# Kernel tuning notes

Hardware: AMD Instinct MI355X
Metric: run time of the kernel (lower is better)

## Reference

```python
import jax, jax.numpy as jnp
import numpy as np

N = 100000      # nodes
E = 1600000     # edges (avg degree 16)
D_IN, D_H, D_OUT = 128, 128, 40
BN_EPS = 1e-5


def _gcn_norm(edge_index):
    # add self-loops, compute symmetric normalization D^-1/2 (A+I) D^-1/2
    loops = jnp.arange(N, dtype=edge_index.dtype)
    src = jnp.concatenate([edge_index[0], loops])
    dst = jnp.concatenate([edge_index[1], loops])
    deg = jax.ops.segment_sum(jnp.ones(src.shape[0], jnp.float32), dst, num_segments=N)
    dinv = jnp.where(deg > 0, jax.lax.rsqrt(deg), 0.0)
    norm = dinv[src] * dinv[dst]  # [E+N]
    return src, dst, norm


def _gcn_conv(h, W, b, src, dst, norm):
    h = h @ W                          # [N, d_out]
    msg = h[src] * norm[:, None]       # [E+N, d_out] gather + scale
    out = jax.ops.segment_sum(msg, dst, num_segments=N)
    return out + b


def _bn(h, g, beta, mean, var):
    return g * (h - mean) * jax.lax.rsqrt(var + BN_EPS) + beta


def setup_inputs() -> dict:
    key = jax.random.key(0)
    ks = jax.random.split(key, 16)
    x = jax.random.normal(ks[0], (N, D_IN), jnp.float32)
    edge_index = jax.random.randint(ks[1], (2, E), 0, N, dtype=jnp.int32)
    s_in, s_h = 1.0 / np.sqrt(D_IN), 1.0 / np.sqrt(D_H)
    W0 = jax.random.normal(ks[2], (D_IN, D_H), jnp.float32) * s_in
    b0 = jnp.zeros((D_H,), jnp.float32)
    W1 = jax.random.normal(ks[3], (D_H, D_H), jnp.float32) * s_h
    b1 = jnp.zeros((D_H,), jnp.float32)
    W2 = jax.random.normal(ks[4], (D_H, D_OUT), jnp.float32) * s_h
    b2 = jnp.zeros((D_OUT,), jnp.float32)
    g0 = jnp.ones((D_H,), jnp.float32)
    be0 = jnp.zeros((D_H,), jnp.float32)
    m0 = jax.random.normal(ks[5], (D_H,), jnp.float32) * 0.1
    v0 = jax.random.uniform(ks[6], (D_H,), jnp.float32) + 0.5
    g1 = jnp.ones((D_H,), jnp.float32)
    be1 = jnp.zeros((D_H,), jnp.float32)
    m1 = jax.random.normal(ks[7], (D_H,), jnp.float32) * 0.1
    v1 = jax.random.uniform(ks[8], (D_H,), jnp.float32) + 0.5
    return {"x": x, "edge_index": edge_index,
            "W0": W0, "b0": b0, "W1": W1, "b1": b1, "W2": W2, "b2": b2,
            "g0": g0, "be0": be0, "m0": m0, "v0": v0,
            "g1": g1, "be1": be1, "m1": m1, "v1": v1}


def reference(x, edge_index, W0, b0, W1, b1, W2, b2,
              g0, be0, m0, v0, g1, be1, m1, v1):
    src, dst, norm = _gcn_norm(edge_index)
    h = _gcn_conv(x, W0, b0, src, dst, norm)
    h = jax.nn.relu(_bn(h, g0, be0, m0, v0))   # dropout = identity in eval
    h = _gcn_conv(h, W1, b1, src, dst, norm)
    h = jax.nn.relu(_bn(h, g1, be1, m1, v1))
    h = _gcn_conv(h, W2, b2, src, dst, norm)
    return jax.nn.log_softmax(h, axis=1)
```

## Files before the change

### kernel.cpp

```cpp
#include <hip/hip_runtime.h>
#include <math.h>


#define CSHIFT 9
#define CSZ 512
#define PCHUNK 8192

typedef unsigned short u16;
typedef unsigned int u32;
typedef unsigned char u8;
typedef float f32x4 __attribute__((ext_vector_type(4)));
typedef short s16x8 __attribute__((ext_vector_type(8)));

__device__ inline float bflo(u32 u) { return __uint_as_float(u << 16); }
__device__ inline float bfhi(u32 u) { return __uint_as_float(u & 0xffff0000u); }
__device__ inline u16 f2bf(float f) {
    u32 b = __float_as_uint(f);
    b += 0x7fff + ((b >> 16) & 1);
    return (u16)(b >> 16);
}
__device__ inline u32 pack2(float lo, float hi) {
    return (u32)f2bf(lo) | ((u32)f2bf(hi) << 16);
}


__global__ __launch_bounds__(256) void k_hist1(const int* __restrict__ dst,
                                               int* __restrict__ hist1,
                                               int E, int NB) {
    __shared__ int h[256];
    int t = threadIdx.x;
    h[t] = 0;
    __syncthreads();
    for (int i = blockIdx.x * 256 * 16 + t; i < min(E, (blockIdx.x + 1) * 256 * 16);
         i += 256)
        atomicAdd(&h[dst[i] >> CSHIFT], 1);
    __syncthreads();
    if (t < NB && h[t]) atomicAdd(&hist1[t], h[t]);
}

__global__ __launch_bounds__(256) void k_scan1(const int* __restrict__ hist1,
                                               int* __restrict__ base1,
                                               int* __restrict__ cur1,
                                               int NB, int E) {
    __shared__ int sc[256];
    int t = threadIdx.x;
    int v = (t < NB) ? hist1[t] : 0;
    sc[t] = v;
    __syncthreads();
    for (int d = 1; d < 256; d <<= 1) {
        int add = (t >= d) ? sc[t - d] : 0;
        __syncthreads();
        sc[t] += add;
        __syncthreads();
    }
    if (t < NB) {
        int excl = sc[t] - v;
        base1[t] = excl;
        cur1[t] = excl;
    }
    if (t == 0) base1[NB] = E;
}

__global__ __launch_bounds__(256) void k_part1(const int* __restrict__ src,
                                               const int* __restrict__ dst,
                                               int* __restrict__ cur1,
                                               u32* __restrict__ bkt,
                                               int E, int NB) {
    __shared__ u32 stage[PCHUNK];
    __shared__ u8 sbin[PCHUNK];
    __shared__ int cnt[256];
    __shared__ int lbase[256];
    __shared__ int lcur[256];
    __shared__ int gb[256];
    int t = threadIdx.x;
    int base = blockIdx.x * PCHUNK;
    int n = min(PCHUNK, E - base);
    cnt[t] = 0;
    __syncthreads();
    for (int i = t; i < n; i += 256) atomicAdd(&cnt[dst[base + i] >> CSHIFT], 1);
    __syncthreads();
    int v = cnt[t];
    lbase[t] = v;
    __syncthreads();
    for (int d = 1; d < 256; d <<= 1) {
        int add = (t >= d) ? lbase[t - d] : 0;
        __syncthreads();
        lbase[t] += add;
        __syncthreads();
    }
    {
        int excl = lbase[t] - v;
        __syncthreads();
        lbase[t] = excl;
        lcur[t] = excl;
        if (t < NB && v) gb[t] = atomicAdd(&cur1[t], v);
    }
    __syncthreads();
    for (int i = t; i < n; i += 256) {
        int d = dst[base + i];
        int s = src[base + i];
        int bin = d >> CSHIFT;
        int p = atomicAdd(&lcur[bin], 1);
        stage[p] = ((u32)s << CSHIFT) | (u32)(d & (CSZ - 1));
        sbin[p] = (u8)bin;
    }
    __syncthreads();
    for (int k = t; k < n; k += 256) {
        int bin = sbin[k];
        bkt[gb[bin] + (k - lbase[bin])] = stage[k];
    }
}

__global__ __launch_bounds__(256) void k_csr(const u32* __restrict__ bkt,
                                             const int* __restrict__ base1,
                                             int* __restrict__ col,
                                             int* __restrict__ row,
                                             float* __restrict__ dinv,
                                             int N, int E) {
    __shared__ int deg[CSZ];
    __shared__ int cur[CSZ];
    __shared__ int sc[256];
    int b = blockIdx.x;
    int t = threadIdx.x;
    int start = base1[b];
    int end = base1[b + 1];
    int nbase = b << CSHIFT;
    deg[t] = 0;
    deg[t + 256] = 0;
    __syncthreads();
    for (int i = start + t; i < end; i += 256)
        atomicAdd(&deg[bkt[i] & (CSZ - 1)], 1);
    __syncthreads();
    int d0 = deg[2 * t], d1 = deg[2 * t + 1];
    int s = d0 + d1;
    sc[t] = s;
    __syncthreads();
    for (int d = 1; d < 256; d <<= 1) {
        int add = (t >= d) ? sc[t - d] : 0;
        __syncthreads();
        sc[t] += add;
        __syncthreads();
    }
    int excl = sc[t] - s;
    cur[2 * t] = excl;
    cur[2 * t + 1] = excl + d0;
    int n0 = nbase + 2 * t, n1 = n0 + 1;
    if (n0 < N) { row[n0] = start + excl;      dinv[n0] = rsqrtf((float)(d0 + 1)); }
    if (n1 < N) { row[n1] = start + excl + d0; dinv[n1] = rsqrtf((float)(d1 + 1)); }
    __syncthreads();
    for (int i = start + t; i < end; i += 256) {
        u32 v = bkt[i];
        int p = start + atomicAdd(&cur[v & (CSZ - 1)], 1);
        col[p] = (int)(v >> CSHIFT);
    }
    if (b == 0 && t == 0) row[N] = E;
}


__global__ __launch_bounds__(256) void k_packW(const float* __restrict__ W,
                                               u16* __restrict__ Wpk) {
    int g = blockIdx.x * 256 + threadIdx.x;
    int j = g & 7;
    int l = (g >> 3) & 63;
    int f = g >> 9;
    int ct = f & 7, ks = f >> 3;
    int krow = ks * 32 + ((l >> 4) << 3) + j;
    int wcol = ct * 16 + (l & 15);
    Wpk[g] = f2bf(W[krow * 128 + wcol]);
}

template <bool AFP32>
__global__ __launch_bounds__(256) void k_gemm128m(const void* __restrict__ Av,
                                                  const u16* __restrict__ Wpk,
                                                  u16* __restrict__ C,
                                                  const float* __restrict__ dinv,
                                                  int M) {
    int tid = threadIdx.x;
    int wv = blockIdx.x * 4 + (tid >> 6);
    int rowbase = wv * 16;
    if (rowbase >= M) return;
    int l = tid & 63;
    int r = l & 15, hi = l >> 4;

    f32x4 acc[8];
#pragma unroll
    for (int ct = 0; ct < 8; ++ct) acc[ct] = (f32x4)(0.f);

    const uint4* wp = (const uint4*)Wpk;
#pragma unroll
    for (int ks = 0; ks < 4; ++ks) {
        s16x8 afrag;
        int abase = (rowbase + r) * 128 + ks * 32 + hi * 8;
        if (AFP32) {
            const float* A = (const float*)Av;
            float4 a0 = *(const float4*)&A[abase];
            float4 a1 = *(const float4*)&A[abase + 4];
            u32 p0 = pack2(a0.x, a0.y), p1 = pack2(a0.z, a0.w);
            u32 p2 = pack2(a1.x, a1.y), p3 = pack2(a1.z, a1.w);
            uint4 u = make_uint4(p0, p1, p2, p3);
            afrag = *(s16x8*)&u;
        } else {
            const u16* A = (const u16*)Av;
            uint4 u = *(const uint4*)&A[abase];
            afrag = *(s16x8*)&u;
        }
#pragma unroll
        for (int ct = 0; ct < 8; ++ct) {
            uint4 b = wp[(ks * 8 + ct) * 64 + l];
            s16x8 bfrag = *(s16x8*)&b;
            acc[ct] = __builtin_amdgcn_mfma_f32_16x16x32_bf16(afrag, bfrag, acc[ct], 0, 0, 0);
        }
    }
    float dv[4];
#pragma unroll
    for (int reg = 0; reg < 4; ++reg) dv[reg] = dinv[rowbase + 4 * hi + reg];
#pragma unroll
    for (int ct = 0; ct < 8; ++ct) {
#pragma unroll
        for (int reg = 0; reg < 4; ++reg) {
            int orow = rowbase + 4 * hi + reg;
            C[(size_t)orow * 128 + ct * 16 + r] = f2bf(dv[reg] * acc[ct][reg]);
        }
    }
}

__global__ __launch_bounds__(256) void k_gemm40(const u16* __restrict__ A,
                                                const float* __restrict__ W,
                                                u16* __restrict__ C,
                                                const float* __restrict__ dinv,
                                                int M) {
    __shared__ float Ws[128 * 40];
    for (int i = threadIdx.x; i < 128 * 40; i += 256) Ws[i] = W[i];
    __syncthreads();
    int r0 = blockIdx.x * 512 + threadIdx.x;
    int r1 = r0 + 256;
    float acc0[40], acc1[40];
#pragma unroll
    for (int c = 0; c < 40; ++c) { acc0[c] = 0.f; acc1[c] = 0.f; }
    const uint2* x0 = (const uint2*)(A + (size_t)min(r0, M - 1) * 128);
    const uint2* x1 = (const uint2*)(A + (size_t)min(r1, M - 1) * 128);
    for (int kb = 0; kb < 32; ++kb) {
        uint2 ua = x0[kb];
        uint2 ub = x1[kb];
        float a0x = bflo(ua.x), a0y = bfhi(ua.x), a0z = bflo(ua.y), a0w = bfhi(ua.y);
        float a1x = bflo(ub.x), a1y = bfhi(ub.x), a1z = bflo(ub.y), a1w = bfhi(ub.y);
        const float* wr = &Ws[kb * 160];
#pragma unroll
        for (int c4 = 0; c4 < 10; ++c4) {
            float4 wk0 = *(const float4*)&wr[c4 * 4];
            float4 wk1 = *(const float4*)&wr[40 + c4 * 4];
            float4 wk2 = *(const float4*)&wr[80 + c4 * 4];
            float4 wk3 = *(const float4*)&wr[120 + c4 * 4];
            int c = c4 * 4;
            acc0[c+0] = fmaf(a0x,wk0.x, fmaf(a0y,wk1.x, fmaf(a0z,wk2.x, fmaf(a0w,wk3.x, acc0[c+0]))));
            acc0[c+1] = fmaf(a0x,wk0.y, fmaf(a0y,wk1.y, fmaf(a0z,wk2.y, fmaf(a0w,wk3.y, acc0[c+1]))));
            acc0[c+2] = fmaf(a0x,wk0.z, fmaf(a0y,wk1.z, fmaf(a0z,wk2.z, fmaf(a0w,wk3.z, acc0[c+2]))));
            acc0[c+3] = fmaf(a0x,wk0.w, fmaf(a0y,wk1.w, fmaf(a0z,wk2.w, fmaf(a0w,wk3.w, acc0[c+3]))));
            acc1[c+0] = fmaf(a1x,wk0.x, fmaf(a1y,wk1.x, fmaf(a1z,wk2.x, fmaf(a1w,wk3.x, acc1[c+0]))));
            acc1[c+1] = fmaf(a1x,wk0.y, fmaf(a1y,wk1.y, fmaf(a1z,wk2.y, fmaf(a1w,wk3.y, acc1[c+1]))));
            acc1[c+2] = fmaf(a1x,wk0.z, fmaf(a1y,wk1.z, fmaf(a1z,wk2.z, fmaf(a1w,wk3.z, acc1[c+2]))));
            acc1[c+3] = fmaf(a1x,wk0.w, fmaf(a1y,wk1.w, fmaf(a1z,wk2.w, fmaf(a1w,wk3.w, acc1[c+3]))));
        }
    }
    if (r0 < M) {
        float s = dinv[r0];
        u32* crow = (u32*)(C + (size_t)r0 * 40);
#pragma unroll
        for (int c2 = 0; c2 < 20; ++c2) crow[c2] = pack2(s * acc0[2*c2], s * acc0[2*c2+1]);
    }
    if (r1 < M) {
        float s = dinv[r1];
        u32* crow = (u32*)(C + (size_t)r1 * 40);
#pragma unroll
        for (int c2 = 0; c2 < 20; ++c2) crow[c2] = pack2(s * acc1[2*c2], s * acc1[2*c2+1]);
    }
}


__global__ __launch_bounds__(256) void k_agg128(const u16* __restrict__ X,
                                                u16* __restrict__ Y,
                                                const int* __restrict__ row,
                                                const int* __restrict__ col,
                                                const float* __restrict__ dinv,
                                                const float* __restrict__ bias,
                                                const float* __restrict__ g,
                                                const float* __restrict__ be,
                                                const float* __restrict__ mean,
                                                const float* __restrict__ var,
                                                int n) {
    int tid = threadIdx.x;
    int wid = tid >> 6, lane = tid & 63;
    int half = lane >> 5, l5 = lane & 31;
    int node = (blockIdx.x * 4 + wid) * 2 + half;
    bool valid = node < n;
    int nc = valid ? node : (n - 1);
    const uint2* xp = (const uint2*)X;
    int s = row[nc], e = row[nc + 1];
    uint2 v = xp[(size_t)nc * 32 + l5];
    float a0 = bflo(v.x), a1 = bfhi(v.x), a2 = bflo(v.y), a3 = bfhi(v.y);
    float b0 = 0, b1 = 0, b2 = 0, b3 = 0;
    float c0 = 0, c1 = 0, c2 = 0, c3 = 0;
    float d0 = 0, d1 = 0, d2 = 0, d3 = 0;
    int j = s;
    for (; j + 8 <= e; j += 8) {
        int e0 = col[j], e1 = col[j+1], e2 = col[j+2], e3 = col[j+3];
        int e4 = col[j+4], e5 = col[j+5], e6 = col[j+6], e7 = col[j+7];
        uint2 x0 = xp[(size_t)e0 * 32 + l5];
        uint2 x1 = xp[(size_t)e1 * 32 + l5];
        uint2 x2 = xp[(size_t)e2 * 32 + l5];
        uint2 x3 = xp[(size_t)e3 * 32 + l5];
        uint2 x4 = xp[(size_t)e4 * 32 + l5];
        uint2 x5 = xp[(size_t)e5 * 32 + l5];
        uint2 x6 = xp[(size_t)e6 * 32 + l5];
        uint2 x7 = xp[(size_t)e7 * 32 + l5];
        a0 += bflo(x0.x); a1 += bfhi(x0.x); a2 += bflo(x0.y); a3 += bfhi(x0.y);
        b0 += bflo(x1.x); b1 += bfhi(x1.x); b2 += bflo(x1.y); b3 += bfhi(x1.y);
        c0 += bflo(x2.x); c1 += bfhi(x2.x); c2 += bflo(x2.y); c3 += bfhi(x2.y);
        d0 += bflo(x3.x); d1 += bfhi(x3.x); d2 += bflo(x3.y); d3 += bfhi(x3.y);
        a0 += bflo(x4.x); a1 += bfhi(x4.x); a2 += bflo(x4.y); a3 += bfhi(x4.y);
        b0 += bflo(x5.x); b1 += bfhi(x5.x); b2 += bflo(x5.y); b3 += bfhi(x5.y);
        c0 += bflo(x6.x); c1 += bfhi(x6.x); c2 += bflo(x6.y); c3 += bfhi(x6.y);
        d0 += bflo(x7.x); d1 += bfhi(x7.x); d2 += bflo(x7.y); d3 += bfhi(x7.y);
    }
    for (; j + 2 <= e; j += 2) {
        int e0 = col[j], e1 = col[j+1];
        uint2 x0 = xp[(size_t)e0 * 32 + l5];
        uint2 x1 = xp[(size_t)e1 * 32 + l5];
        a0 += bflo(x0.x); a1 += bfhi(x0.x); a2 += bflo(x0.y); a3 += bfhi(x0.y);
        b0 += bflo(x1.x); b1 += bfhi(x1.x); b2 += bflo(x1.y); b3 += bfhi(x1.y);
    }
    if (j < e) {
        uint2 x0 = xp[(size_t)col[j] * 32 + l5];
        c0 += bflo(x0.x); c1 += bfhi(x0.x); c2 += bflo(x0.y); c3 += bfhi(x0.y);
    }
    float dv = dinv[nc];
    float s0 = dv * ((a0 + b0) + (c0 + d0));
    float s1 = dv * ((a1 + b1) + (c1 + d1));
    float s2 = dv * ((a2 + b2) + (c2 + d2));
    float s3 = dv * ((a3 + b3) + (c3 + d3));
    float4 g4 = ((const float4*)g)[l5];
    float4 be4 = ((const float4*)be)[l5];
    float4 m4 = ((const float4*)mean)[l5];
    float4 v4 = ((const float4*)var)[l5];
    float4 bi4 = ((const float4*)bias)[l5];
    float sc0 = g4.x * rsqrtf(v4.x + 1e-5f);
    float sc1 = g4.y * rsqrtf(v4.y + 1e-5f);
    float sc2 = g4.z * rsqrtf(v4.z + 1e-5f);
    float sc3 = g4.w * rsqrtf(v4.w + 1e-5f);
    float y0 = fmaxf(fmaf(sc0, s0, fmaf(sc0, bi4.x - m4.x, be4.x)), 0.f);
    float y1 = fmaxf(fmaf(sc1, s1, fmaf(sc1, bi4.y - m4.y, be4.y)), 0.f);
    float y2 = fmaxf(fmaf(sc2, s2, fmaf(sc2, bi4.z - m4.z, be4.z)), 0.f);
    float y3 = fmaxf(fmaf(sc3, s3, fmaf(sc3, bi4.w - m4.w, be4.w)), 0.f);
    if (valid) {
        uint2 o;
        o.x = pack2(y0, y1);
        o.y = pack2(y2, y3);
        ((uint2*)Y)[(size_t)node * 32 + l5] = o;
    }
}

__global__ __launch_bounds__(256) void k_agg40(const u16* __restrict__ X,
                                               float* __restrict__ out,
                                               const int* __restrict__ row,
                                               const int* __restrict__ col,
                                               const float* __restrict__ dinv,
                                               const float* __restrict__ b2,
                                               int n) {
    int tid = threadIdx.x;
    int wid = tid >> 6, lane = tid & 63;
    int half = lane >> 5, l5 = lane & 31;
    int node = (blockIdx.x * 4 + wid) * 2 + half;
    bool valid = node < n;
    int nc = valid ? node : (n - 1);
    bool active = l5 < 20;
    const u32* xp = (const u32*)X;
    int s = row[nc], e = row[nc + 1];
    float a0 = 0, a1 = 0, b0 = 0, b1 = 0, c0 = 0, c1 = 0, d0 = 0, d1 = 0;
    if (active) {
        u32 v = xp[(size_t)nc * 20 + l5];
        a0 = bflo(v); a1 = bfhi(v);
    }
    int j = s;
    for (; j + 8 <= e; j += 8) {
        int e0 = col[j], e1 = col[j+1], e2 = col[j+2], e3 = col[j+3];
        int e4 = col[j+4], e5 = col[j+5], e6 = col[j+6], e7 = col[j+7];
        if (active) {
            u32 x0 = xp[(size_t)e0 * 20 + l5];
            u32 x1 = xp[(size_t)e1 * 20 + l5];
            u32 x2 = xp[(size_t)e2 * 20 + l5];
            u32 x3 = xp[(size_t)e3 * 20 + l5];
            u32 x4 = xp[(size_t)e4 * 20 + l5];
            u32 x5 = xp[(size_t)e5 * 20 + l5];
            u32 x6 = xp[(size_t)e6 * 20 + l5];
            u32 x7 = xp[(size_t)e7 * 20 + l5];
            a0 += bflo(x0); a1 += bfhi(x0);
            b0 += bflo(x1); b1 += bfhi(x1);
            c0 += bflo(x2); c1 += bfhi(x2);
            d0 += bflo(x3); d1 += bfhi(x3);
            a0 += bflo(x4); a1 += bfhi(x4);
            b0 += bflo(x5); b1 += bfhi(x5);
            c0 += bflo(x6); c1 += bfhi(x6);
            d0 += bflo(x7); d1 += bfhi(x7);
        }
    }
    for (; j + 2 <= e; j += 2) {
        int e0 = col[j], e1 = col[j+1];
        if (active) {
            u32 x0 = xp[(size_t)e0 * 20 + l5];
            u32 x1 = xp[(size_t)e1 * 20 + l5];
            a0 += bflo(x0); a1 += bfhi(x0);
            b0 += bflo(x1); b1 += bfhi(x1);
        }
    }
    if (j < e && active) {
        u32 x0 = xp[(size_t)col[j] * 20 + l5];
        c0 += bflo(x0); c1 += bfhi(x0);
    }
    float dv = dinv[nc];
    float ylo = -INFINITY, yhi = -INFINITY;
    if (active) {
        float2 bb = ((const float2*)b2)[l5];
        ylo = fmaf(dv, (a0 + b0) + (c0 + d0), bb.x);
        yhi = fmaf(dv, (a1 + b1) + (c1 + d1), bb.y);
    }
    float m = fmaxf(ylo, yhi);
#pragma unroll
    for (int d = 16; d; d >>= 1) m = fmaxf(m, __shfl_xor(m, d));
    float ex = active ? (__expf(ylo - m) + __expf(yhi - m)) : 0.f;
#pragma unroll
    for (int d = 16; d; d >>= 1) ex += __shfl_xor(ex, d);
    if (valid && active) {
        float lse = m + __logf(ex);
        ((float2*)out)[(size_t)node * 20 + l5] = make_float2(ylo - lse, yhi - lse);
    }
}


extern "C" void kernel_launch(void* const* d_in, const int* in_sizes, int n_in,
                              void* d_out, int out_size, void* d_ws, size_t ws_size,
                              hipStream_t stream) {
    const float* x   = (const float*)d_in[0];
    const int*   ei  = (const int*)d_in[1];
    const float* W0  = (const float*)d_in[2];
    const float* b0  = (const float*)d_in[3];
    const float* W1  = (const float*)d_in[4];
    const float* b1  = (const float*)d_in[5];
    const float* W2  = (const float*)d_in[6];
    const float* b2  = (const float*)d_in[7];
    const float* g0  = (const float*)d_in[8];
    const float* be0 = (const float*)d_in[9];
    const float* m0  = (const float*)d_in[10];
    const float* v0  = (const float*)d_in[11];
    const float* g1  = (const float*)d_in[12];
    const float* be1 = (const float*)d_in[13];
    const float* m1  = (const float*)d_in[14];
    const float* v1  = (const float*)d_in[15];
    float* out = (float*)d_out;

    int N = in_sizes[0] / 128;
    int E = in_sizes[1] / 2;
    const int* src = ei;
    const int* dst = ei + E;

    int NB = (N + CSZ - 1) / CSZ;

    char* ws = (char*)d_ws;
    size_t off = 0;
    auto alloc = [&](size_t bytes) -> char* {
        char* p = ws + off;
        off += (bytes + 255) & ~(size_t)255;
        return p;
    };
    u16*   XsA   = (u16*)alloc((size_t)N * 128 * 2);
    u16*   hB    = (u16*)alloc((size_t)N * 128 * 2);
    u16*   bufC  = (u16*)alloc((size_t)N * 40 * 2);
    int*   col   = (int*)alloc((size_t)E * 4);
    int*   row   = (int*)alloc((size_t)(N + 1) * 4);
    float* dinv  = (float*)alloc((size_t)N * 4);
    int*   hist1 = (int*)alloc((size_t)(NB + 1) * 4);
    int*   base1 = (int*)alloc((size_t)(NB + 1) * 4);
    int*   cur1  = (int*)alloc((size_t)(NB + 1) * 4);
    u16*   Wpk0  = (u16*)alloc(128 * 128 * 2);
    u16*   Wpk1  = (u16*)alloc(128 * 128 * 2);
    u32*   bkt   = (u32*)XsA;

    hipMemsetAsync(hist1, 0, (size_t)(NB + 1) * 4, stream);
    k_hist1<<<(E + 4095) / 4096, 256, 0, stream>>>(dst, hist1, E, NB);
    k_scan1<<<1, 256, 0, stream>>>(hist1, base1, cur1, NB, E);
    k_part1<<<(E + PCHUNK - 1) / PCHUNK, 256, 0, stream>>>(src, dst, cur1, bkt, E, NB);
    k_csr<<<NB, 256, 0, stream>>>(bkt, base1, col, row, dinv, N, E);
    k_packW<<<64, 256, 0, stream>>>(W0, Wpk0);
    k_packW<<<64, 256, 0, stream>>>(W1, Wpk1);

    int gemmGrid = ((N + 15) / 16 + 3) / 4;
    k_gemm128m<true><<<gemmGrid, 256, 0, stream>>>(x, Wpk0, XsA, dinv, N);
    k_agg128<<<(N + 7) / 8, 256, 0, stream>>>(XsA, hB, row, col, dinv, b0, g0, be0, m0, v0, N);
    k_gemm128m<false><<<gemmGrid, 256, 0, stream>>>(hB, Wpk1, XsA, dinv, N);
    k_agg128<<<(N + 7) / 8, 256, 0, stream>>>(XsA, hB, row, col, dinv, b1, g1, be1, m1, v1, N);
    k_gemm40<<<(N + 511) / 512, 256, 0, stream>>>(hB, W2, bufC, dinv, N);
    k_agg40<<<(N + 7) / 8, 256, 0, stream>>>(bufC, out, row, col, dinv, b2, N);
}
```

Measured before the change: 315.7 us.

## Fuse aggregation+BN+ReLU with the following layer's GEMM via LDS-staged MFMA

Merges each 128-wide aggregation kernel with the next layer's weight GEMM. Each block aggregates 16 nodes, applies bias, BN and ReLU, writes the bf16 rows to a swizzled LDS tile, then runs MFMA on it against packed weights. This removes the round trip of the intermediate hidden matrix through global memory and two launches. The last GEMM now uses MFMA with weights zero-padded to 48 columns instead of a scalar FMA kernel. The cost is lower occupancy from 512-thread blocks with a barrier, and only some waves do the MFMA work.

Result: faster. 284.8 us (-9.8%).

```diff
diff --git a/kernel.cpp b/kernel.cpp
--- a/kernel.cpp
+++ b/kernel.cpp
@@ -169,12 +169,25 @@
     Wpk[g] = f2bf(W[krow * 128 + wcol]);
 }
 
-template <bool AFP32>
-__global__ __launch_bounds__(256) void k_gemm128m(const void* __restrict__ Av,
-                                                  const u16* __restrict__ Wpk,
-                                                  u16* __restrict__ C,
-                                                  const float* __restrict__ dinv,
-                                                  int M) {
+__global__ __launch_bounds__(256) void k_packW40(const float* __restrict__ W,
+                                                 u16* __restrict__ Wpk) {
+    int g = blockIdx.x * 256 + threadIdx.x;
+    if (g >= 12 * 512) return;
+    int j = g & 7;
+    int l = (g >> 3) & 63;
+    int f = g >> 9;
+    int ct = f % 3, ks = f / 3;
+    int krow = ks * 32 + ((l >> 4) << 3) + j;
+    int wcol = ct * 16 + (l & 15);
+    Wpk[g] = (wcol < 40) ? f2bf(W[krow * 40 + wcol]) : (u16)0;
+}
+
+
+__global__ __launch_bounds__(256) void k_gemm0(const float* __restrict__ A,
+                                               const u16* __restrict__ Wpk,
+                                               u16* __restrict__ C,
+                                               const float* __restrict__ dinv,
+                                               int M) {
     int tid = threadIdx.x;
     int wv = blockIdx.x * 4 + (tid >> 6);
     int rowbase = wv * 16;
@@ -189,21 +202,12 @@
     const uint4* wp = (const uint4*)Wpk;
 #pragma unroll
     for (int ks = 0; ks < 4; ++ks) {
-        s16x8 afrag;
-        int abase = (rowbase + r) * 128 + ks * 32 + hi * 8;
-        if (AFP32) {
-            const float* A = (const float*)Av;
-            float4 a0 = *(const float4*)&A[abase];
-            float4 a1 = *(const float4*)&A[abase + 4];
-            u32 p0 = pack2(a0.x, a0.y), p1 = pack2(a0.z, a0.w);
-            u32 p2 = pack2(a1.x, a1.y), p3 = pack2(a1.z, a1.w);
-            uint4 u = make_uint4(p0, p1, p2, p3);
-            afrag = *(s16x8*)&u;
-        } else {
-            const u16* A = (const u16*)Av;
-            uint4 u = *(const uint4*)&A[abase];
-            afrag = *(s16x8*)&u;
-        }
+        int abase = (min(rowbase + r, M - 1)) * 128 + ks * 32 + hi * 8;
+        float4 a0 = *(const float4*)&A[abase];
+        float4 a1 = *(const float4*)&A[abase + 4];
+        uint4 u = make_uint4(pack2(a0.x, a0.y), pack2(a0.z, a0.w),
+                             pack2(a1.x, a1.y), pack2(a1.z, a1.w));
+        s16x8 afrag = *(s16x8*)&u;
 #pragma unroll
         for (int ct = 0; ct < 8; ++ct) {
             uint4 b = wp[(ks * 8 + ct) * 64 + l];
@@ -213,89 +217,44 @@
     }
     float dv[4];
 #pragma unroll
-    for (int reg = 0; reg < 4; ++reg) dv[reg] = dinv[rowbase + 4 * hi + reg];
+    for (int reg = 0; reg < 4; ++reg) {
+        int orow = rowbase + 4 * hi + reg;
+        dv[reg] = (orow < M) ? dinv[orow] : 0.f;
+    }
 #pragma unroll
     for (int ct = 0; ct < 8; ++ct) {
 #pragma unroll
         for (int reg = 0; reg < 4; ++reg) {
             int orow = rowbase + 4 * hi + reg;
-            C[(size_t)orow * 128 + ct * 16 + r] = f2bf(dv[reg] * acc[ct][reg]);
+            if (orow < M)
+                C[(size_t)orow * 128 + ct * 16 + r] = f2bf(dv[reg] * acc[ct][reg]);
         }
     }
 }
 
-__global__ __launch_bounds__(256) void k_gemm40(const u16* __restrict__ A,
-                                                const float* __restrict__ W,
-                                                u16* __restrict__ C,
-                                                const float* __restrict__ dinv,
-                                                int M) {
-    __shared__ float Ws[128 * 40];
-    for (int i = threadIdx.x; i < 128 * 40; i += 256) Ws[i] = W[i];
-    __syncthreads();
-    int r0 = blockIdx.x * 512 + threadIdx.x;
-    int r1 = r0 + 256;
-    float acc0[40], acc1[40];
-#pragma unroll
-    for (int c = 0; c < 40; ++c) { acc0[c] = 0.f; acc1[c] = 0.f; }
-    const uint2* x0 = (const uint2*)(A + (size_t)min(r0, M - 1) * 128);
-    const uint2* x1 = (const uint2*)(A + (size_t)min(r1, M - 1) * 128);
-    for (int kb = 0; kb < 32; ++kb) {
-        uint2 ua = x0[kb];
-        uint2 ub = x1[kb];
-        float a0x = bflo(ua.x), a0y = bfhi(ua.x), a0z = bflo(ua.y), a0w = bfhi(ua.y);
-        float a1x = bflo(ub.x), a1y = bfhi(ub.x), a1z = bflo(ub.y), a1w = bfhi(ub.y);
-        const float* wr = &Ws[kb * 160];
-#pragma unroll
-        for (int c4 = 0; c4 < 10; ++c4) {
-            float4 wk0 = *(const float4*)&wr[c4 * 4];
-            float4 wk1 = *(const float4*)&wr[40 + c4 * 4];
-            float4 wk2 = *(const float4*)&wr[80 + c4 * 4];
-            float4 wk3 = *(const float4*)&wr[120 + c4 * 4];
-            int c = c4 * 4;
-            acc0[c+0] = fmaf(a0x,wk0.x, fmaf(a0y,wk1.x, fmaf(a0z,wk2.x, fmaf(a0w,wk3.x, acc0[c+0]))));
-            acc0[c+1] = fmaf(a0x,wk0.y, fmaf(a0y,wk1.y, fmaf(a0z,wk2.y, fmaf(a0w,wk3.y, acc0[c+1]))));
-            acc0[c+2] = fmaf(a0x,wk0.z, fmaf(a0y,wk1.z, fmaf(a0z,wk2.z, fmaf(a0w,wk3.z, acc0[c+2]))));
-            acc0[c+3] = fmaf(a0x,wk0.w, fmaf(a0y,wk1.w, fmaf(a0z,wk2.w, fmaf(a0w,wk3.w, acc0[c+3]))));
-            acc1[c+0] = fmaf(a1x,wk0.x, fmaf(a1y,wk1.x, fmaf(a1z,wk2.x, fmaf(a1w,wk3.x, acc1[c+0]))));
-            acc1[c+1] = fmaf(a1x,wk0.y, fmaf(a1y,wk1.y, fmaf(a1z,wk2.y, fmaf(a1w,wk3.y, acc1[c+1]))));
-            acc1[c+2] = fmaf(a1x,wk0.z, fmaf(a1y,wk1.z, fmaf(a1z,wk2.z, fmaf(a1w,wk3.z, acc1[c+2]))));
-            acc1[c+3] = fmaf(a1x,wk0.w, fmaf(a1y,wk1.w, fmaf(a1z,wk2.w, fmaf(a1w,wk3.w, acc1[c+3]))));
-        }
-    }
-    if (r0 < M) {
-        float s = dinv[r0];
-        u32* crow = (u32*)(C + (size_t)r0 * 40);
-#pragma unroll
-        for (int c2 = 0; c2 < 20; ++c2) crow[c2] = pack2(s * acc0[2*c2], s * acc0[2*c2+1]);
-    }
-    if (r1 < M) {
-        float s = dinv[r1];
-        u32* crow = (u32*)(C + (size_t)r1 * 40);
-#pragma unroll
-        for (int c2 = 0; c2 < 20; ++c2) crow[c2] = pack2(s * acc1[2*c2], s * acc1[2*c2+1]);
-    }
-}
-
-
-__global__ __launch_bounds__(256) void k_agg128(const u16* __restrict__ X,
-                                                u16* __restrict__ Y,
-                                                const int* __restrict__ row,
-                                                const int* __restrict__ col,
-                                                const float* __restrict__ dinv,
-                                                const float* __restrict__ bias,
-                                                const float* __restrict__ g,
-                                                const float* __restrict__ be,
-                                                const float* __restrict__ mean,
-                                                const float* __restrict__ var,
-                                                int n) {
+
+template <int NCT>
+__global__ __launch_bounds__(512) void k_fused(const u16* __restrict__ X,
+                                               const u16* __restrict__ Wpk,
+                                               u16* __restrict__ O,
+                                               const int* __restrict__ row,
+                                               const int* __restrict__ col,
+                                               const float* __restrict__ dinv,
+                                               const float* __restrict__ bias,
+                                               const float* __restrict__ g,
+                                               const float* __restrict__ be,
+                                               const float* __restrict__ mean,
+                                               const float* __restrict__ var,
+                                               int n, int ostride) {
+    __shared__ u32 hl[16][64];
     int tid = threadIdx.x;
-    int wid = tid >> 6, lane = tid & 63;
-    int half = lane >> 5, l5 = lane & 31;
-    int node = (blockIdx.x * 4 + wid) * 2 + half;
-    bool valid = node < n;
-    int nc = valid ? node : (n - 1);
+    int nl = tid >> 5;
+    int l5 = tid & 31;
+    int node = blockIdx.x * 16 + nl;
+    int nc = min(node, n - 1);
     const uint2* xp = (const uint2*)X;
     int s = row[nc], e = row[nc + 1];
+
     uint2 v = xp[(size_t)nc * 32 + l5];
     float a0 = bflo(v.x), a1 = bfhi(v.x), a2 = bflo(v.y), a3 = bfhi(v.y);
     float b0 = 0, b1 = 0, b2 = 0, b3 = 0;
@@ -333,11 +292,11 @@
         uint2 x0 = xp[(size_t)col[j] * 32 + l5];
         c0 += bflo(x0.x); c1 += bfhi(x0.x); c2 += bflo(x0.y); c3 += bfhi(x0.y);
     }
-    float dv = dinv[nc];
-    float s0 = dv * ((a0 + b0) + (c0 + d0));
-    float s1 = dv * ((a1 + b1) + (c1 + d1));
-    float s2 = dv * ((a2 + b2) + (c2 + d2));
-    float s3 = dv * ((a3 + b3) + (c3 + d3));
+    float dvn = dinv[nc];
+    float s0 = dvn * ((a0 + b0) + (c0 + d0));
+    float s1 = dvn * ((a1 + b1) + (c1 + d1));
+    float s2 = dvn * ((a2 + b2) + (c2 + d2));
+    float s3 = dvn * ((a3 + b3) + (c3 + d3));
     float4 g4 = ((const float4*)g)[l5];
     float4 be4 = ((const float4*)be)[l5];
     float4 m4 = ((const float4*)mean)[l5];
@@ -351,13 +310,39 @@
     float y1 = fmaxf(fmaf(sc1, s1, fmaf(sc1, bi4.y - m4.y, be4.y)), 0.f);
     float y2 = fmaxf(fmaf(sc2, s2, fmaf(sc2, bi4.z - m4.z, be4.z)), 0.f);
     float y3 = fmaxf(fmaf(sc3, s3, fmaf(sc3, bi4.w - m4.w, be4.w)), 0.f);
-    if (valid) {
-        uint2 o;
-        o.x = pack2(y0, y1);
-        o.y = pack2(y2, y3);
-        ((uint2*)Y)[(size_t)node * 32 + l5] = o;
-    }
-}
+    {
+        int unit = (l5 >> 1) ^ nl;
+        uint2* p = (uint2*)&hl[nl][(unit << 2) + ((l5 & 1) << 1)];
+        *p = make_uint2(pack2(y0, y1), pack2(y2, y3));
+    }
+    __syncthreads();
+
+    int w = tid >> 6;
+    if (w < NCT) {
+        int l = tid & 63;
+        int r = l & 15, hi = l >> 4;
+        f32x4 acc = (f32x4)(0.f);
+        const uint4* wp = (const uint4*)Wpk;
+#pragma unroll
+        for (int ks = 0; ks < 4; ++ks) {
+            int unit = (ks * 4 + hi) ^ r;
+            uint4 a = *(const uint4*)&hl[r][unit << 2];
+            s16x8 afrag = *(s16x8*)&a;
+            uint4 b = wp[(ks * NCT + w) * 64 + l];
+            s16x8 bfrag = *(s16x8*)&b;
+            acc = __builtin_amdgcn_mfma_f32_16x16x32_bf16(afrag, bfrag, acc, 0, 0, 0);
+        }
+        int nbase = blockIdx.x * 16;
+#pragma unroll
+        for (int reg = 0; reg < 4; ++reg) {
+            int orow = nbase + 4 * hi + reg;
+            int oc = w * 16 + r;
+            if (orow < n && (NCT == 8 || oc < 40))
+                O[(size_t)orow * ostride + oc] = f2bf(dinv[orow] * acc[reg]);
+        }
+    }
+}
+
 
 __global__ __launch_bounds__(256) void k_agg40(const u16* __restrict__ X,
                                                float* __restrict__ out,
@@ -375,45 +360,42 @@
     bool active = l5 < 20;
     const u32* xp = (const u32*)X;
     int s = row[nc], e = row[nc + 1];
+    int li = min(l5, 19);
     float a0 = 0, a1 = 0, b0 = 0, b1 = 0, c0 = 0, c1 = 0, d0 = 0, d1 = 0;
-    if (active) {
-        u32 v = xp[(size_t)nc * 20 + l5];
+    {
+        u32 v = xp[(size_t)nc * 20 + li];
         a0 = bflo(v); a1 = bfhi(v);
     }
     int j = s;
     for (; j + 8 <= e; j += 8) {
         int e0 = col[j], e1 = col[j+1], e2 = col[j+2], e3 = col[j+3];
         int e4 = col[j+4], e5 = col[j+5], e6 = col[j+6], e7 = col[j+7];
-        if (active) {
-            u32 x0 = xp[(size_t)e0 * 20 + l5];
-            u32 x1 = xp[(size_t)e1 * 20 + l5];
-            u32 x2 = xp[(size_t)e2 * 20 + l5];
-            u32 x3 = xp[(size_t)e3 * 20 + l5];
-            u32 x4 = xp[(size_t)e4 * 20 + l5];
-            u32 x5 = xp[(size_t)e5 * 20 + l5];
-            u32 x6 = xp[(size_t)e6 * 20 + l5];
-            u32 x7 = xp[(size_t)e7 * 20 + l5];
-            a0 += bflo(x0); a1 += bfhi(x0);
-            b0 += bflo(x1); b1 += bfhi(x1);
-            c0 += bflo(x2); c1 += bfhi(x2);
-            d0 += bflo(x3); d1 += bfhi(x3);
-            a0 += bflo(x4); a1 += bfhi(x4);
-            b0 += bflo(x5); b1 += bfhi(x5);
-            c0 += bflo(x6); c1 += bfhi(x6);
-            d0 += bflo(x7); d1 += bfhi(x7);
-        }
+        u32 x0 = xp[(size_t)e0 * 20 + li];
+        u32 x1 = xp[(size_t)e1 * 20 + li];
+        u32 x2 = xp[(size_t)e2 * 20 + li];
+        u32 x3 = xp[(size_t)e3 * 20 + li];
+        u32 x4 = xp[(size_t)e4 * 20 + li];
+        u32 x5 = xp[(size_t)e5 * 20 + li];
+        u32 x6 = xp[(size_t)e6 * 20 + li];
+        u32 x7 = xp[(size_t)e7 * 20 + li];
+        a0 += bflo(x0); a1 += bfhi(x0);
+        b0 += bflo(x1); b1 += bfhi(x1);
+        c0 += bflo(x2); c1 += bfhi(x2);
+        d0 += bflo(x3); d1 += bfhi(x3);
+        a0 += bflo(x4); a1 += bfhi(x4);
+        b0 += bflo(x5); b1 += bfhi(x5);
+        c0 += bflo(x6); c1 += bfhi(x6);
+        d0 += bflo(x7); d1 += bfhi(x7);
     }
     for (; j + 2 <= e; j += 2) {
         int e0 = col[j], e1 = col[j+1];
-        if (active) {
-            u32 x0 = xp[(size_t)e0 * 20 + l5];
-            u32 x1 = xp[(size_t)e1 * 20 + l5];
-            a0 += bflo(x0); a1 += bfhi(x0);
-            b0 += bflo(x1); b1 += bfhi(x1);
-        }
-    }
-    if (j < e && active) {
-        u32 x0 = xp[(size_t)col[j] * 20 + l5];
+        u32 x0 = xp[(size_t)e0 * 20 + li];
+        u32 x1 = xp[(size_t)e1 * 20 + li];
+        a0 += bflo(x0); a1 += bfhi(x0);
+        b0 += bflo(x1); b1 += bfhi(x1);
+    }
+    if (j < e) {
+        u32 x0 = xp[(size_t)col[j] * 20 + li];
         c0 += bflo(x0); c1 += bfhi(x0);
     }
     float dv = dinv[nc];
@@ -472,9 +454,9 @@
         return p;
     };
     u16*   XsA   = (u16*)alloc((size_t)N * 128 * 2);
-    u16*   hB    = (u16*)alloc((size_t)N * 128 * 2);
+    u16*   XsB   = (u16*)alloc((size_t)N * 128 * 2);
     u16*   bufC  = (u16*)alloc((size_t)N * 40 * 2);
-    int*   col   = (int*)alloc((size_t)E * 4);
+    int*   col   = (int*)alloc((size_t)E * 4 + 64);
     int*   row   = (int*)alloc((size_t)(N + 1) * 4);
     float* dinv  = (float*)alloc((size_t)N * 4);
     int*   hist1 = (int*)alloc((size_t)(NB + 1) * 4);
@@ -482,6 +464,7 @@
     int*   cur1  = (int*)alloc((size_t)(NB + 1) * 4);
     u16*   Wpk0  = (u16*)alloc(128 * 128 * 2);
     u16*   Wpk1  = (u16*)alloc(128 * 128 * 2);
+    u16*   Wpk2  = (u16*)alloc(128 * 48 * 2);
     u32*   bkt   = (u32*)XsA;
 
     hipMemsetAsync(hist1, 0, (size_t)(NB + 1) * 4, stream);
@@ -491,12 +474,14 @@
     k_csr<<<NB, 256, 0, stream>>>(bkt, base1, col, row, dinv, N, E);
     k_packW<<<64, 256, 0, stream>>>(W0, Wpk0);
     k_packW<<<64, 256, 0, stream>>>(W1, Wpk1);
+    k_packW40<<<24, 256, 0, stream>>>(W2, Wpk2);
 
     int gemmGrid = ((N + 15) / 16 + 3) / 4;
-    k_gemm128m<true><<<gemmGrid, 256, 0, stream>>>(x, Wpk0, XsA, dinv, N);
-    k_agg128<<<(N + 7) / 8, 256, 0, stream>>>(XsA, hB, row, col, dinv, b0, g0, be0, m0, v0, N);
-    k_gemm128m<false><<<gemmGrid, 256, 0, stream>>>(hB, Wpk1, XsA, dinv, N);
-    k_agg128<<<(N + 7) / 8, 256, 0, stream>>>(XsA, hB, row, col, dinv, b1, g1, be1, m1, v1, N);
-    k_gemm40<<<(N + 511) / 512, 256, 0, stream>>>(hB, W2, bufC, dinv, N);
+    k_gemm0<<<gemmGrid, 256, 0, stream>>>(x, Wpk0, XsA, dinv, N);
+    int fusedGrid = (N + 15) / 16;
+    k_fused<8><<<fusedGrid, 512, 0, stream>>>(XsA, Wpk1, XsB, row, col, dinv,
+                                              b0, g0, be0, m0, v0, N, 128);
+    k_fused<3><<<fusedGrid, 512, 0, stream>>>(XsB, Wpk2, bufC, row, col, dinv,
+                                              b1, g1, be1, m1, v1, N, 40);
     k_agg40<<<(N + 7) / 8, 256, 0, stream>>>(bufC, out, row, col, dinv, b2, N);
 }
```
